# Performance work log

Measured on AMD Instinct MI355X. Metric: run time of the kernel, lower is better.

The kernel has to match this reference:

```python
import jax, jax.numpy as jnp
import numpy as np

B, H, W, C = 4, 128, 128, 256
APL = 3  # anchors per location


def setup_inputs() -> dict:
    key = jax.random.key(0)
    ks = jax.random.split(key, 4)
    inputs = jax.random.normal(ks[0], (B, H, W, C), dtype=jnp.float32)
    # he_normal-ish scaled weights
    w_shared = jax.random.normal(ks[1], (3, 3, C, 512), dtype=jnp.float32) * (2.0 / (3 * 3 * C)) ** 0.5
    b_shared = jnp.zeros((512,), dtype=jnp.float32)
    w_cls = jax.random.normal(ks[2], (1, 1, 512, 2 * APL), dtype=jnp.float32) * (2.0 / 512) ** 0.5
    b_cls = jnp.zeros((2 * APL,), dtype=jnp.float32)
    w_delta = jax.random.normal(ks[3], (1, 1, 512, 4 * APL), dtype=jnp.float32) * (2.0 / 512) ** 0.5
    b_delta = jnp.zeros((4 * APL,), dtype=jnp.float32)
    return {"inputs": inputs, "w_shared": w_shared, "b_shared": b_shared,
            "w_cls": w_cls, "b_cls": b_cls, "w_delta": w_delta, "b_delta": b_delta}


def reference(inputs, w_shared, b_shared, w_cls, b_cls, w_delta, b_delta):
    # rpn_conv_shared: 3x3 SAME conv -> ReLU
    shared = jax.lax.conv_general_dilated(
        inputs, w_shared, window_strides=(1, 1), padding='SAME',
        dimension_numbers=('NHWC', 'HWIO', 'NHWC')) + b_shared
    shared = jax.nn.relu(shared)
    b = inputs.shape[0]
    # 1x1 convs are just per-pixel matmuls
    cls = jnp.einsum('bhwc,co->bhwo', shared, w_cls[0, 0]) + b_cls
    rpn_class_logits = cls.reshape(b, -1, 2)  # [B, num_anchors, 2]
    rpn_probs = jax.nn.softmax(rpn_class_logits, axis=-1)
    dlt = jnp.einsum('bhwc,co->bhwo', shared, w_delta[0, 0]) + b_delta
    rpn_deltas = dlt.reshape(b, -1, 4)  # [B, num_anchors, 4]
    return (rpn_class_logits, rpn_probs, rpn_deltas)
```

## Files before the change

kernel.cpp:

```cpp
#include <hip/hip_runtime.h>
#include <stdint.h>

#define BATCH 4
#define HH 128
#define WW 128
#define CIN 256
#define CO 512
#define HP 130
#define NPIX (BATCH*HH*WW)
#define LOGITS_N (NPIX*6)
#define DELTA_BASE (2*LOGITS_N)

typedef short bf16x8 __attribute__((ext_vector_type(8)));
typedef unsigned short u16x8 __attribute__((ext_vector_type(8)));
typedef float f32x4 __attribute__((ext_vector_type(4)));
typedef unsigned int u32;

__device__ __forceinline__ unsigned short f2bf(float f) {
    union { float f; unsigned int u; } v; v.f = f;
    return (unsigned short)((v.u + 0x7FFFu + ((v.u >> 16) & 1u)) >> 16);
}

__device__ __forceinline__ void gload16(const unsigned short* g, char* l) {
    __builtin_amdgcn_global_load_lds(
        (const __attribute__((address_space(1))) u32*)g,
        (__attribute__((address_space(3))) u32*)l, 16, 0, 0);
}

__global__ __launch_bounds__(256) void k_pad_convert(const float* __restrict__ in,
                                                     unsigned short* __restrict__ out) {
    size_t q = (size_t)blockIdx.x*256 + threadIdx.x;
    if (q >= (size_t)BATCH*HP*HP*64) return;
    int c4 = ((int)q & 63) * 4;
    int pix = (int)(q >> 6);
    int xx = pix % HP; int t = pix / HP; int yy = t % HP; int b = t / HP;
    ushort4 r = {0, 0, 0, 0};
    if (yy >= 1 && yy <= HH && xx >= 1 && xx <= WW) {
        const float4 v = *(const float4*)(in + (((size_t)(b*HH) + (yy-1))*WW + (xx-1))*CIN + c4);
        r.x = f2bf(v.x); r.y = f2bf(v.y); r.z = f2bf(v.z); r.w = f2bf(v.w);
    }
    *(ushort4*)(out + (size_t)pix*CIN + c4) = r;
}

__global__ __launch_bounds__(256) void k_wt_convert(const float* __restrict__ w,
                                                    unsigned short* __restrict__ wt) {
    int n = blockIdx.x % CO; int tap = blockIdx.x / CO;
    int c = threadIdx.x;
    wt[((size_t)tap*CO + n)*CIN + c] = f2bf(w[((size_t)tap*CIN + c)*CO + n]);
}

__global__ __launch_bounds__(512, 2) void k_main8(
    const unsigned short* __restrict__ in_p,
    const unsigned short* __restrict__ wt,
    const float* __restrict__ b_sh,
    const float* __restrict__ w_cls,
    const float* __restrict__ w_dlt,
    float* __restrict__ part)
{
    extern __shared__ char LDS[];
    char* const BBASE = LDS + 98304;

    const int tid  = threadIdx.x;
    const int lane = tid & 63, wave = tid >> 6;
    const int l15  = lane & 15, l4 = lane >> 4;
    const int wm   = wave >> 2, wn = wave & 3;

    const int bid   = ((blockIdx.x & 7) << 6) + (blockIdx.x >> 3);
    const int ntile = bid & 1, mtile = bid >> 1;
    const int n0 = ntile << 8;
    const int b  = mtile >> 6;
    const int y0 = (mtile & 63) * 2;

    const int rl0 = tid >> 3, pc0 = tid & 7;
    const int kc0 = pc0 ^ (rl0 & 7);
    const int off = rl0*256 + kc0*8;
    const int t16 = tid*16;

    int base_a[2], base_b[2];
    #pragma unroll
    for (int kk = 0; kk < 2; kk++) {
        int swz = ((kk*32 + l4*8)*2) ^ ((l15 & 7) << 4);
        base_a[kk] = (wm*128 + l15)*128 + swz;
        base_b[kk] = (wn*64 + l15)*128 + swz;
    }

    f32x4 acc[8][4];
    const f32x4 zz = {0.f, 0.f, 0.f, 0.f};
    #pragma unroll
    for (int mi = 0; mi < 8; mi++)
        #pragma unroll
        for (int ni = 0; ni < 4; ni++) acc[mi][ni] = zz;

    {
        const unsigned short* gA0 = in_p + ((size_t)(b*HP + y0))*HP*256;
        const unsigned short* gB0 = wt + (size_t)n0*256;
        const unsigned short* gA1 = gA0 + 64;
        gload16(gA0 + off,          LDS + t16);
        gload16(gA0 + 16384 + off,  LDS + 8192 + t16);
        gload16(gA0 + 33280 + off,  LDS + 16384 + t16);
        gload16(gA0 + 49664 + off,  LDS + 24576 + t16);
        __builtin_amdgcn_sched_barrier(0);
        gload16(gB0 + off,          BBASE + t16);
        gload16(gB0 + 16384 + off,  BBASE + 8192 + t16);
        gload16(gB0 + 32768 + off,  BBASE + 16384 + t16);
        gload16(gB0 + 49152 + off,  BBASE + 24576 + t16);
        __builtin_amdgcn_sched_barrier(0);
        gload16(gA1 + off,          LDS + 32768 + t16);
        gload16(gA1 + 16384 + off,  LDS + 40960 + t16);
        gload16(gA1 + 33280 + off,  LDS + 49152 + t16);
        gload16(gA1 + 49664 + off,  LDS + 57344 + t16);
    }
    asm volatile("s_waitcnt vmcnt(4)" ::: "memory");
    __builtin_amdgcn_sched_barrier(0);
    __builtin_amdgcn_s_barrier();
    __builtin_amdgcn_sched_barrier(0);

#define MFMA_Q(Q, AQ)                                                        \
    __builtin_amdgcn_s_setprio(1);                                           \
    _Pragma("unroll")                                                        \
    for (int kk = 0; kk < 2; kk++)                                           \
        _Pragma("unroll")                                                    \
        for (int mm = 0; mm < 2; mm++)                                       \
            _Pragma("unroll")                                                \
            for (int ni = 0; ni < 4; ni++)                                   \
                acc[2*(Q)+mm][ni] = __builtin_amdgcn_mfma_f32_16x16x32_bf16( \
                    AQ[mm][kk], breg[ni][kk], acc[2*(Q)+mm][ni], 0, 0, 0);   \
    __builtin_amdgcn_s_setprio(0);

#define LOAD_Q(AQ, Q)                                                        \
    _Pragma("unroll")                                                        \
    for (int kk = 0; kk < 2; kk++) {                                         \
        AQ[0][kk] = *(const bf16x8*)(bufA + base_a[kk] + (2*(Q))*2048);      \
        AQ[1][kk] = *(const bf16x8*)(bufA + base_a[kk] + (2*(Q)+1)*2048);    \
    }

    int ia = 0;
    for (int s = 0; s < 36; ++s) {
        const int s1 = s + 1;
        const int tapB = s1 >> 2, kqB = s1 & 3;
        const unsigned short* gB = wt + ((size_t)(tapB*512 + n0))*256 + kqB*64;
        const int s2p = s + 2;
        const int tapA = s2p >> 2, kqA = s2p & 3;
        const int dyA = (tapA*11) >> 5, dxA = tapA - dyA*3;
        const unsigned short* gA = in_p + ((size_t)((b*HP + y0 + dyA)*HP + dxA))*256 + kqA*64;

        const char* bufA = LDS + (ia << 15);
        const char* bufB = BBASE + ((s & 1) << 15);
        int iw = ia + 2; if (iw > 2) iw -= 3;
        char* Ad = LDS + (iw << 15);
        char* Bd = BBASE + ((s1 & 1) << 15);
        const bool moreB = (s < 35), moreA = (s < 34);

        bf16x8 breg[4][2];
        #pragma unroll
        for (int kk = 0; kk < 2; kk++) {
            breg[0][kk] = *(const bf16x8*)(bufB + base_b[kk]);
            breg[1][kk] = *(const bf16x8*)(bufB + base_b[kk] + 2048);
            breg[2][kk] = *(const bf16x8*)(bufB + base_b[kk] + 4096);
            breg[3][kk] = *(const bf16x8*)(bufB + base_b[kk] + 6144);
        }
        bf16x8 a0[2][2], a1[2][2], a2[2][2], a3[2][2];
        LOAD_Q(a0, 0)
        __builtin_amdgcn_sched_barrier(0);
        if (moreB) {
            gload16(gB + off,          Bd + t16);
            gload16(gB + 16384 + off,  Bd + 8192 + t16);
            gload16(gB + 32768 + off,  Bd + 16384 + t16);
            gload16(gB + 49152 + off,  Bd + 24576 + t16);
        }
        __builtin_amdgcn_sched_barrier(0);
        LOAD_Q(a1, 1)
        MFMA_Q(0, a0)
        LOAD_Q(a2, 2)
        if (moreA) {
            gload16(gA + off,          Ad + t16);
            gload16(gA + 16384 + off,  Ad + 8192 + t16);
            gload16(gA + 33280 + off,  Ad + 16384 + t16);
            gload16(gA + 49664 + off,  Ad + 24576 + t16);
        }
        __builtin_amdgcn_sched_barrier(0);
        MFMA_Q(1, a1)
        LOAD_Q(a3, 3)
        MFMA_Q(2, a2)
        MFMA_Q(3, a3)

        if (moreA)      { asm volatile("s_waitcnt vmcnt(4)" ::: "memory"); }
        else if (moreB) { asm volatile("s_waitcnt vmcnt(0)" ::: "memory"); }
        __builtin_amdgcn_sched_barrier(0);
        __builtin_amdgcn_s_barrier();
        __builtin_amdgcn_sched_barrier(0);

        ia = ia == 2 ? 0 : ia + 1;
    }
#undef MFMA_Q
#undef LOAD_Q

    float* shf = (float*)LDS;
    float* sW  = (float*)(LDS + 66560);
    for (int j = tid; j < 256*18; j += 512) {
        int c = j / 18, o = j - c*18;
        sW[c*20 + o] = (o < 6) ? w_cls[(size_t)(n0 + c)*6 + o]
                               : w_dlt[(size_t)(n0 + c)*12 + (o - 6)];
    }
    float bsh[4];
    #pragma unroll
    for (int ni = 0; ni < 4; ni++) bsh[ni] = b_sh[n0 + wn*64 + ni*16 + l15];

    float a18[18];
    #pragma unroll
    for (int o = 0; o < 18; o++) a18[o] = 0.f;
    const int rr = tid & 255, chalf = tid >> 8;
    __syncthreads();

    for (int p = 0; p < 4; ++p) {
        if (wn == p) {
            #pragma unroll
            for (int mi = 0; mi < 8; mi++)
                #pragma unroll
                for (int ni = 0; ni < 4; ni++) {
                    int colL = ni*16 + l15;
                    int row0 = wm*128 + mi*16 + l4*4;
                    f32x4 v = acc[mi][ni];
                    f32x4 sv;
                    #pragma unroll
                    for (int r = 0; r < 4; r++) sv[r] = fmaxf(v[r] + bsh[ni], 0.f);
                    *(f32x4*)(shf + colL*260 + row0) = sv;
                }
        }
        __syncthreads();
        #pragma unroll 4
        for (int i = 0; i < 32; i++) {
            int c = chalf*32 + i;
            float v = shf[c*260 + rr];
            const float* wrow = sW + (p*64 + c)*20;
            #pragma unroll
            for (int o = 0; o < 18; o++) a18[o] += v * wrow[o];
        }
        __syncthreads();
    }

    if (chalf == 1) {
        #pragma unroll
        for (int o = 0; o < 18; o++) shf[rr*18 + o] = a18[o];
    }
    __syncthreads();
    if (chalf == 0) {
        float* dst = part + ((size_t)ntile*NPIX + (size_t)mtile*256 + rr)*18;
        #pragma unroll
        for (int o = 0; o < 18; o++) dst[o] = a18[o] + shf[rr*18 + o];
    }
}

__global__ __launch_bounds__(256) void k_finalize_ws(const float* __restrict__ part,
                                                     float* __restrict__ out,
                                                     const float* __restrict__ b_cls,
                                                     const float* __restrict__ b_dlt) {
    int pix = blockIdx.x*256 + threadIdx.x;
    if (pix >= NPIX) return;
    float s[18];
    #pragma unroll
    for (int o = 0; o < 18; o++)
        s[o] = part[(size_t)pix*18 + o] + part[((size_t)NPIX + pix)*18 + o];
    float* lo = out + (size_t)pix*6;
    float* pr = out + (size_t)LOGITS_N + (size_t)pix*6;
    float* dl = out + (size_t)DELTA_BASE + (size_t)pix*12;
    #pragma unroll
    for (int a = 0; a < 3; a++) {
        float l0 = s[a*2]   + b_cls[a*2];
        float l1 = s[a*2+1] + b_cls[a*2+1];
        lo[a*2] = l0; lo[a*2+1] = l1;
        float m = fmaxf(l0, l1);
        float e0 = __expf(l0 - m), e1 = __expf(l1 - m);
        float inv = 1.f / (e0 + e1);
        pr[a*2] = e0*inv; pr[a*2+1] = e1*inv;
    }
    #pragma unroll
    for (int o = 0; o < 12; o++) dl[o] = s[6 + o] + b_dlt[o];
}

__global__ __launch_bounds__(256) void k_main_fb(
    const float* __restrict__ in_f, const float* __restrict__ w_f,
    const float* __restrict__ b_sh, const float* __restrict__ w_cls,
    const float* __restrict__ w_dlt, float* __restrict__ out)
{
    __shared__ float smemf[11008];
    char* smem  = (char*)smemf;
    char* smemB = smem + 16384;
    const int tid = threadIdx.x;
    const int lane = tid & 63, wave = tid >> 6;
    const int l15 = lane & 15, l4 = lane >> 4;
    const int wr = wave >> 1, wc = wave & 1;
    int bid = ((blockIdx.x & 7) << 8) + (blockIdx.x >> 3);
    const int ntile = bid & 3, mtile = bid >> 2;
    const int n0 = ntile << 7;
    const int b = mtile >> 7, y = mtile & 127;
    int aoff[4][2], boff[4][2];
    #pragma unroll
    for (int mi = 0; mi < 4; mi++) {
        int rowA = wr*64 + mi*16 + l15;
        int rowB = wc*64 + mi*16 + l15;
        #pragma unroll
        for (int kk = 0; kk < 2; kk++) {
            int kb = (kk*32 + l4*8) * 2;
            aoff[mi][kk] = rowA*128 + (kb ^ ((rowA & 7) << 4));
            boff[mi][kk] = rowB*128 + (kb ^ ((rowB & 7) << 4));
        }
    }
    f32x4 acc[4][4];
    const f32x4 zz = {0.f, 0.f, 0.f, 0.f};
    #pragma unroll
    for (int mi = 0; mi < 4; mi++)
        #pragma unroll
        for (int ni = 0; ni < 4; ni++) acc[mi][ni] = zz;
    for (int s = 0; s < 36; s++) {
        int tap = s >> 2, kq = s & 3;
        int dy = tap / 3, dx = tap - dy*3;
        const int c0 = kq * 64;
        const int yy = y + dy - 1;
        const bool yok = (yy >= 0) && (yy < HH);
        #pragma unroll
        for (int i = 0; i < 4; i++) {
            int ci = i*256 + tid;
            int row = ci >> 3, pc = ci & 7;
            int kc = pc ^ (row & 7);
            int xx = row + dx - 1;
            u16x8 a;
            if (yok && xx >= 0 && xx < WW) {
                const float* sp = in_f + (((size_t)(b*HH) + yy)*WW + xx)*CIN + c0 + kc*8;
                #pragma unroll
                for (int j = 0; j < 8; j++) a[j] = (short)f2bf(sp[j]);
            } else {
                #pragma unroll
                for (int j = 0; j < 8; j++) a[j] = 0;
            }
            *(u16x8*)(smem + ci*16) = a;
            const float* wsrc = w_f + ((size_t)(tap*CIN + c0 + kc*8))*CO + n0 + row;
            u16x8 bb;
            #pragma unroll
            for (int j = 0; j < 8; j++) bb[j] = (short)f2bf(wsrc[(size_t)j*CO]);
            *(u16x8*)(smemB + ci*16) = bb;
        }
        __syncthreads();
        #pragma unroll
        for (int kk = 0; kk < 2; kk++) {
            bf16x8 av[4], bv[4];
            #pragma unroll
            for (int mi = 0; mi < 4; mi++) av[mi] = *(const bf16x8*)(smem  + aoff[mi][kk]);
            #pragma unroll
            for (int ni = 0; ni < 4; ni++) bv[ni] = *(const bf16x8*)(smemB + boff[ni][kk]);
            #pragma unroll
            for (int mi = 0; mi < 4; mi++)
                #pragma unroll
                for (int ni = 0; ni < 4; ni++)
                    acc[mi][ni] = __builtin_amdgcn_mfma_f32_16x16x32_bf16(
                        av[mi], bv[ni], acc[mi][ni], 0, 0, 0);
        }
        __syncthreads();
    }
    float* shf = smemf;
    float* sW  = smemf + 8448;
    for (int j = tid; j < 128*18; j += 256) {
        int c = j / 18, o = j - c*18;
        sW[c*20 + o] = (o < 6) ? w_cls[(size_t)(n0 + c)*6 + o]
                               : w_dlt[(size_t)(n0 + c)*12 + (o - 6)];
    }
    float bsh[4];
    #pragma unroll
    for (int ni = 0; ni < 4; ni++) bsh[ni] = b_sh[n0 + wc*64 + ni*16 + l15];
    float a18[18];
    #pragma unroll
    for (int o = 0; o < 18; o++) a18[o] = 0.f;
    const int rr = tid & 127, chalf = tid >> 7;
    #pragma unroll
    for (int pass = 0; pass < 2; pass++) {
        if (wc == pass) {
            #pragma unroll
            for (int mi = 0; mi < 4; mi++)
                #pragma unroll
                for (int ni = 0; ni < 4; ni++) {
                    int colL = ni*16 + l15;
                    int row0 = wr*64 + mi*16 + l4*4;
                    f32x4 v = acc[mi][ni];
                    f32x4 sv;
                    #pragma unroll
                    for (int r = 0; r < 4; r++) sv[r] = fmaxf(v[r] + bsh[ni], 0.f);
                    *(f32x4*)(shf + colL*132 + row0) = sv;
                }
        }
        __syncthreads();
        #pragma unroll 4
        for (int i = 0; i < 32; i++) {
            int c = chalf*32 + i;
            float v = shf[c*132 + rr];
            const float* wrow = sW + (pass*64 + c)*20;
            #pragma unroll
            for (int o = 0; o < 18; o++) a18[o] += v * wrow[o];
        }
        __syncthreads();
    }
    const int pixel = mtile*128 + rr;
    float* lo = out + (size_t)pixel*6;
    float* dl = out + DELTA_BASE + (size_t)pixel*12;
    #pragma unroll
    for (int o = 0; o < 6; o++)  atomicAdd(lo + o, a18[o]);
    #pragma unroll
    for (int o = 0; o < 12; o++) atomicAdd(dl + o, a18[6 + o]);
}

__global__ __launch_bounds__(256) void k_finalize(float* __restrict__ out,
                                                  const float* __restrict__ b_cls,
                                                  const float* __restrict__ b_dlt) {
    int pix = blockIdx.x*256 + threadIdx.x;
    if (pix >= NPIX) return;
    float* lo = out + (size_t)pix*6;
    float* pr = out + (size_t)LOGITS_N + (size_t)pix*6;
    float* dl = out + (size_t)DELTA_BASE + (size_t)pix*12;
    #pragma unroll
    for (int a = 0; a < 3; a++) {
        float l0 = lo[a*2]   + b_cls[a*2];
        float l1 = lo[a*2+1] + b_cls[a*2+1];
        lo[a*2] = l0; lo[a*2+1] = l1;
        float m = fmaxf(l0, l1);
        float e0 = __expf(l0 - m), e1 = __expf(l1 - m);
        float inv = 1.f / (e0 + e1);
        pr[a*2] = e0*inv; pr[a*2+1] = e1*inv;
    }
    #pragma unroll
    for (int o = 0; o < 12; o++) dl[o] += b_dlt[o];
}

extern "C" void kernel_launch(void* const* d_in, const int* in_sizes, int n_in,
                              void* d_out, int out_size, void* d_ws, size_t ws_size,
                              hipStream_t stream) {
    const float* in    = (const float*)d_in[0];
    const float* w_sh  = (const float*)d_in[1];
    const float* b_sh  = (const float*)d_in[2];
    const float* w_cls = (const float*)d_in[3];
    const float* b_cls = (const float*)d_in[4];
    const float* w_dlt = (const float*)d_in[5];
    const float* b_dlt = (const float*)d_in[6];
    float* out = (float*)d_out;

    const size_t in_p_elems = (size_t)BATCH*HP*HP*CIN;
    const size_t wt_elems   = (size_t)9*CO*CIN;
    const size_t part_elems = (size_t)2*NPIX*18;
    const size_t need = (in_p_elems + wt_elems)*2 + part_elems*4;

    if (ws_size >= need) {
        unsigned short* in_p = (unsigned short*)d_ws;
        unsigned short* wt   = in_p + in_p_elems;
        float* part = (float*)(wt + wt_elems);
        hipFuncSetAttribute((const void*)k_main8,
                            hipFuncAttributeMaxDynamicSharedMemorySize, 163840);
        int padq = (int)(((size_t)BATCH*HP*HP*64 + 255)/256);
        k_pad_convert<<<padq, 256, 0, stream>>>(in, in_p);
        k_wt_convert<<<9*CO, 256, 0, stream>>>(w_sh, wt);
        k_main8<<<512, 512, 163840, stream>>>(in_p, wt, b_sh, w_cls, w_dlt, part);
        k_finalize_ws<<<(NPIX + 255)/256, 256, 0, stream>>>(part, out, b_cls, b_dlt);
    } else {
        hipMemsetAsync(d_out, 0, (size_t)out_size * sizeof(float), stream);
        k_main_fb<<<2048, 256, 0, stream>>>(in, w_sh, b_sh, w_cls, w_dlt, out);
        k_finalize<<<(NPIX + 255)/256, 256, 0, stream>>>(out, b_cls, b_dlt);
    }
}
```

Baseline: 192.5 us.

## Load conv weights directly from global into registers, dropping LDS staging

The weight (B) operand is no longer double-buffered through LDS via async global-to-LDS copies. Each wave now loads its B fragments straight from global memory into registers at the start of every k-step. The MFMAs are split into two half-K phases, each gated by a vmcnt wait. This frees 64KB of LDS and removes the B LDS reads, but puts global-load latency on the critical path with no prefetch and relies on L1/L2 for reuse across waves.

Measured after the change: 287.2 us. +49.2%, slower.

```diff
diff --git a/kernel.cpp b/kernel.cpp
--- a/kernel.cpp
+++ b/kernel.cpp
@@ -58,7 +58,6 @@
     float* __restrict__ part)
 {
     extern __shared__ char LDS[];
-    char* const BBASE = LDS + 98304;
 
     const int tid  = threadIdx.x;
     const int lane = tid & 63, wave = tid >> 6;
@@ -76,13 +75,14 @@
     const int off = rl0*256 + kc0*8;
     const int t16 = tid*16;
 
-    int base_a[2], base_b[2];
+    int base_a[2];
     #pragma unroll
     for (int kk = 0; kk < 2; kk++) {
         int swz = ((kk*32 + l4*8)*2) ^ ((l15 & 7) << 4);
         base_a[kk] = (wm*128 + l15)*128 + swz;
-        base_b[kk] = (wn*64 + l15)*128 + swz;
-    }
+    }
+
+    const unsigned short* gBl = wt + (size_t)(n0 + wn*64 + l15)*256 + l4*8;
 
     f32x4 acc[8][4];
     const f32x4 zz = {0.f, 0.f, 0.f, 0.f};
@@ -93,18 +93,12 @@
 
     {
         const unsigned short* gA0 = in_p + ((size_t)(b*HP + y0))*HP*256;
-        const unsigned short* gB0 = wt + (size_t)n0*256;
         const unsigned short* gA1 = gA0 + 64;
         gload16(gA0 + off,          LDS + t16);
         gload16(gA0 + 16384 + off,  LDS + 8192 + t16);
         gload16(gA0 + 33280 + off,  LDS + 16384 + t16);
         gload16(gA0 + 49664 + off,  LDS + 24576 + t16);
         __builtin_amdgcn_sched_barrier(0);
-        gload16(gB0 + off,          BBASE + t16);
-        gload16(gB0 + 16384 + off,  BBASE + 8192 + t16);
-        gload16(gB0 + 32768 + off,  BBASE + 16384 + t16);
-        gload16(gB0 + 49152 + off,  BBASE + 24576 + t16);
-        __builtin_amdgcn_sched_barrier(0);
         gload16(gA1 + off,          LDS + 32768 + t16);
         gload16(gA1 + 16384 + off,  LDS + 40960 + t16);
         gload16(gA1 + 33280 + off,  LDS + 49152 + t16);
@@ -114,18 +108,6 @@
     __builtin_amdgcn_sched_barrier(0);
     __builtin_amdgcn_s_barrier();
     __builtin_amdgcn_sched_barrier(0);
-
-#define MFMA_Q(Q, AQ)                                                        \
-    __builtin_amdgcn_s_setprio(1);                                           \
-    _Pragma("unroll")                                                        \
-    for (int kk = 0; kk < 2; kk++)                                           \
-        _Pragma("unroll")                                                    \
-        for (int mm = 0; mm < 2; mm++)                                       \
-            _Pragma("unroll")                                                \
-            for (int ni = 0; ni < 4; ni++)                                   \
-                acc[2*(Q)+mm][ni] = __builtin_amdgcn_mfma_f32_16x16x32_bf16( \
-                    AQ[mm][kk], breg[ni][kk], acc[2*(Q)+mm][ni], 0, 0, 0);   \
-    __builtin_amdgcn_s_setprio(0);
 
 #define LOAD_Q(AQ, Q)                                                        \
     _Pragma("unroll")                                                        \
@@ -134,44 +116,41 @@
         AQ[1][kk] = *(const bf16x8*)(bufA + base_a[kk] + (2*(Q)+1)*2048);    \
     }
 
+#define MFMA_K(Q, AQ, KK, BREG)                                              \
+    __builtin_amdgcn_s_setprio(1);                                           \
+    _Pragma("unroll")                                                        \
+    for (int mm = 0; mm < 2; mm++)                                           \
+        _Pragma("unroll")                                                    \
+        for (int ni = 0; ni < 4; ni++)                                       \
+            acc[2*(Q)+mm][ni] = __builtin_amdgcn_mfma_f32_16x16x32_bf16(     \
+                AQ[mm][KK], BREG[ni], acc[2*(Q)+mm][ni], 0, 0, 0);           \
+    __builtin_amdgcn_s_setprio(0);
+
     int ia = 0;
     for (int s = 0; s < 36; ++s) {
-        const int s1 = s + 1;
-        const int tapB = s1 >> 2, kqB = s1 & 3;
-        const unsigned short* gB = wt + ((size_t)(tapB*512 + n0))*256 + kqB*64;
+        const int tap0 = s >> 2, kq0 = s & 3;
+        const unsigned short* gB = gBl + (size_t)tap0*131072 + kq0*64;
         const int s2p = s + 2;
         const int tapA = s2p >> 2, kqA = s2p & 3;
         const int dyA = (tapA*11) >> 5, dxA = tapA - dyA*3;
         const unsigned short* gA = in_p + ((size_t)((b*HP + y0 + dyA)*HP + dxA))*256 + kqA*64;
 
         const char* bufA = LDS + (ia << 15);
-        const char* bufB = BBASE + ((s & 1) << 15);
         int iw = ia + 2; if (iw > 2) iw -= 3;
         char* Ad = LDS + (iw << 15);
-        char* Bd = BBASE + ((s1 & 1) << 15);
-        const bool moreB = (s < 35), moreA = (s < 34);
-
-        bf16x8 breg[4][2];
-        #pragma unroll
-        for (int kk = 0; kk < 2; kk++) {
-            breg[0][kk] = *(const bf16x8*)(bufB + base_b[kk]);
-            breg[1][kk] = *(const bf16x8*)(bufB + base_b[kk] + 2048);
-            breg[2][kk] = *(const bf16x8*)(bufB + base_b[kk] + 4096);
-            breg[3][kk] = *(const bf16x8*)(bufB + base_b[kk] + 6144);
-        }
+        const bool moreA = (s < 34);
+
+        bf16x8 breg0[4], breg1[4];
+        #pragma unroll
+        for (int ni = 0; ni < 4; ni++) breg0[ni] = *(const bf16x8*)(gB + ni*4096);
+        #pragma unroll
+        for (int ni = 0; ni < 4; ni++) breg1[ni] = *(const bf16x8*)(gB + 32 + ni*4096);
+        __builtin_amdgcn_sched_barrier(0);
+
         bf16x8 a0[2][2], a1[2][2], a2[2][2], a3[2][2];
         LOAD_Q(a0, 0)
-        __builtin_amdgcn_sched_barrier(0);
-        if (moreB) {
-            gload16(gB + off,          Bd + t16);
-            gload16(gB + 16384 + off,  Bd + 8192 + t16);
-            gload16(gB + 32768 + off,  Bd + 16384 + t16);
-            gload16(gB + 49152 + off,  Bd + 24576 + t16);
-        }
-        __builtin_amdgcn_sched_barrier(0);
         LOAD_Q(a1, 1)
-        MFMA_Q(0, a0)
-        LOAD_Q(a2, 2)
+        __builtin_amdgcn_sched_barrier(0);
         if (moreA) {
             gload16(gA + off,          Ad + t16);
             gload16(gA + 16384 + off,  Ad + 8192 + t16);
@@ -179,21 +158,33 @@
             gload16(gA + 49664 + off,  Ad + 24576 + t16);
         }
         __builtin_amdgcn_sched_barrier(0);
-        MFMA_Q(1, a1)
+        LOAD_Q(a2, 2)
         LOAD_Q(a3, 3)
-        MFMA_Q(2, a2)
-        MFMA_Q(3, a3)
-
-        if (moreA)      { asm volatile("s_waitcnt vmcnt(4)" ::: "memory"); }
-        else if (moreB) { asm volatile("s_waitcnt vmcnt(0)" ::: "memory"); }
+
+        if (moreA) { asm volatile("s_waitcnt vmcnt(8)" ::: "memory"); }
+        else       { asm volatile("s_waitcnt vmcnt(4)" ::: "memory"); }
+        __builtin_amdgcn_sched_barrier(0);
+        MFMA_K(0, a0, 0, breg0)
+        MFMA_K(1, a1, 0, breg0)
+        MFMA_K(2, a2, 0, breg0)
+        MFMA_K(3, a3, 0, breg0)
+
+        if (moreA) { asm volatile("s_waitcnt vmcnt(4)" ::: "memory"); }
+        else       { asm volatile("s_waitcnt vmcnt(0)" ::: "memory"); }
+        __builtin_amdgcn_sched_barrier(0);
+        MFMA_K(0, a0, 1, breg1)
+        MFMA_K(1, a1, 1, breg1)
+        MFMA_K(2, a2, 1, breg1)
+        MFMA_K(3, a3, 1, breg1)
+
         __builtin_amdgcn_sched_barrier(0);
         __builtin_amdgcn_s_barrier();
         __builtin_amdgcn_sched_barrier(0);
 
         ia = ia == 2 ? 0 : ia + 1;
     }
-#undef MFMA_Q
 #undef LOAD_Q
+#undef MFMA_K
 
     float* shf = (float*)LDS;
     float* sW  = (float*)(LDS + 66560);
@@ -451,11 +442,11 @@
         unsigned short* wt   = in_p + in_p_elems;
         float* part = (float*)(wt + wt_elems);
         hipFuncSetAttribute((const void*)k_main8,
-                            hipFuncAttributeMaxDynamicSharedMemorySize, 163840);
+                            hipFuncAttributeMaxDynamicSharedMemorySize, 98304);
         int padq = (int)(((size_t)BATCH*HP*HP*64 + 255)/256);
         k_pad_convert<<<padq, 256, 0, stream>>>(in, in_p);
         k_wt_convert<<<9*CO, 256, 0, stream>>>(w_sh, wt);
-        k_main8<<<512, 512, 163840, stream>>>(in_p, wt, b_sh, w_cls, w_dlt, part);
+        k_main8<<<512, 512, 98304, stream>>>(in_p, wt, b_sh, w_cls, w_dlt, part);
         k_finalize_ws<<<(NPIX + 255)/256, 256, 0, stream>>>(part, out, b_cls, b_dlt);
     } else {
         hipMemsetAsync(d_out, 0, (size_t)out_size * sizeof(float), stream);
```
